# Kernel tuning notes

Hardware: AMD Instinct MI355X
Metric: run time of the kernel (lower is better)

## Reference

```python
import math
import jax, jax.numpy as jnp
import numpy as np

E = 1024
H = 16
D = E // H  # head_dim = 64
B, T = 4, 2048


def setup_inputs() -> dict:
    key = jax.random.key(0)
    ks = jax.random.split(key, 9)
    s = 1.0 / math.sqrt(E)
    inp = {
        "x": jax.random.normal(ks[0], (B, T, E), dtype=jnp.float32),
        "Wq": jax.random.uniform(ks[1], (E, E), jnp.float32, -s, s),
        "bq": jax.random.uniform(ks[2], (E,), jnp.float32, -s, s),
        "Wk": jax.random.uniform(ks[3], (E, E), jnp.float32, -s, s),
        "bk": jax.random.uniform(ks[4], (E,), jnp.float32, -s, s),
        "Wv": jax.random.uniform(ks[5], (E, E), jnp.float32, -s, s),
        "bv": jax.random.uniform(ks[6], (E,), jnp.float32, -s, s),
        "Wo": jax.random.uniform(ks[7], (E, E), jnp.float32, -s, s),
        "bo": jax.random.uniform(ks[8], (E,), jnp.float32, -s, s),
    }
    return inp


def reference(x, Wq, bq, Wk, bk, Wv, bv, Wo, bo):
    # Linear projections (torch Linear: y = x @ W.T + b)
    q = x @ Wq.T + bq
    k = x @ Wk.T + bk
    v = x @ Wv.T + bv
    # [B, T, E] -> [B, H, T, D]
    def split_heads(t):
        return t.reshape(B, T, H, D).transpose(0, 2, 1, 3)
    q, k, v = split_heads(q), split_heads(k), split_heads(v)
    # scaled dot-product attention; note scale uses head_dim (attention(self.head_dim))
    scores = jnp.einsum("bhqd,bhkd->bhqk", q, k) / math.sqrt(D)
    attn = jax.nn.softmax(scores, axis=-1)
    out = jnp.einsum("bhqk,bhkd->bhqd", attn, v)
    out = out.transpose(0, 2, 1, 3).reshape(B, T, E)
    return out @ Wo.T + bo
```

## Files before the change

### kernel.cpp

```cpp
#include <hip/hip_runtime.h>

typedef short bh8 __attribute__((ext_vector_type(8)));
typedef short bh4 __attribute__((ext_vector_type(4)));
typedef float f4 __attribute__((ext_vector_type(4)));
typedef _Float16 fh4 __attribute__((ext_vector_type(4)));
typedef __fp16 hp2 __attribute__((ext_vector_type(2)));
typedef unsigned int u32;

#if __has_builtin(__builtin_amdgcn_exp2f)
#define EXP2(x) __builtin_amdgcn_exp2f(x)
#else
#define EXP2(x) exp2f(x)
#endif

__device__ __forceinline__ short f2bf(float f) {
  unsigned u = __float_as_uint(f);
  u += 0x7FFFu + ((u >> 16) & 1u);
  return (short)(u >> 16);
}

__device__ __forceinline__ short f2fh(float f) {
  union { hp2 h2; u32 u; } cv;
  cv.h2 = __builtin_amdgcn_cvt_pkrtz(f, f);
  return (short)(cv.u & 0xffffu);
}

__device__ __forceinline__ void async16(const void* g, void* l) {
  __builtin_amdgcn_global_load_lds((const __attribute__((address_space(1))) void*)g,
                                   (__attribute__((address_space(3))) void*)l, 16, 0, 0);
}

__global__ void cvt_kernel(const float* __restrict__ in, short* __restrict__ out, int n4) {
  int i = blockIdx.x * blockDim.x + threadIdx.x;
  if (i < n4) {
    f4 v = *(const f4*)(in + (size_t)i * 4);
    bh4 o;
    o[0] = f2bf(v[0]); o[1] = f2bf(v[1]); o[2] = f2bf(v[2]); o[3] = f2bf(v[3]);
    *(bh4*)(out + (size_t)i * 4) = o;
  }
}

__global__ void cvt_w4(const float* __restrict__ w0, const float* __restrict__ w1,
                       const float* __restrict__ w2, const float* __restrict__ w3,
                       short* __restrict__ out, int n4_per) {
  const float* in = blockIdx.y == 0 ? w0 : blockIdx.y == 1 ? w1 : blockIdx.y == 2 ? w2 : w3;
  short* o = out + (size_t)blockIdx.y * (size_t)n4_per * 4;
  int i = blockIdx.x * blockDim.x + threadIdx.x;
  if (i < n4_per) {
    f4 v = *(const f4*)(in + (size_t)i * 4);
    bh4 q;
    q[0] = f2bf(v[0]); q[1] = f2bf(v[1]); q[2] = f2bf(v[2]); q[3] = f2bf(v[3]);
    *(bh4*)(o + (size_t)i * 4) = q;
  }
}

template <typename OutT, bool BROW, bool F16OUT>
__device__ __forceinline__ void gemm_body(const short* __restrict__ A, const short* __restrict__ Bw,
                                          const float* __restrict__ bias, OutT* __restrict__ C,
                                          int m0, int n0, int N, int K, float scale,
                                          short* a_lds, short* b_lds) {
  const int t = threadIdx.x;
  const int lane = t & 63, wave = t >> 6, quad = lane >> 4, l15 = lane & 15;
  const int mw = (wave >> 1) * 64, nw = (wave & 1) * 64;

  f4 acc[4][4];
#pragma unroll
  for (int i = 0; i < 4; ++i)
#pragma unroll
    for (int j = 0; j < 4; ++j) acc[i][j] = (f4){0.f, 0.f, 0.f, 0.f};

  for (int k0 = 0; k0 < K; k0 += 64) {
#pragma unroll
    for (int i = 0; i < 4; ++i) {
      int c = i * 256 + t;
      int m = c >> 3;
      int kq = (c & 7) ^ (m & 7);
      const short* ga = A + (size_t)(m0 + m) * K + k0 + kq * 8;
      const short* gb = Bw + (size_t)(n0 + m) * K + k0 + kq * 8;
      async16(ga, (char*)a_lds + (i * 256 + wave * 64) * 16);
      async16(gb, (char*)b_lds + (i * 256 + wave * 64) * 16);
    }
    __syncthreads();
#pragma unroll
    for (int s = 0; s < 2; ++s) {
      bh8 af[4], bfr[4];
#pragma unroll
      for (int ms = 0; ms < 4; ++ms) {
        int m = mw + ms * 16 + l15;
        int slot = m * 8 + ((quad + s * 4) ^ (m & 7));
        af[ms] = *(const bh8*)(a_lds + slot * 8);
      }
#pragma unroll
      for (int ns = 0; ns < 4; ++ns) {
        int n = nw + ns * 16 + l15;
        int slot = n * 8 + ((quad + s * 4) ^ (n & 7));
        bfr[ns] = *(const bh8*)(b_lds + slot * 8);
      }
#pragma unroll
      for (int ms = 0; ms < 4; ++ms)
#pragma unroll
        for (int ns = 0; ns < 4; ++ns)
          acc[ms][ns] = __builtin_amdgcn_mfma_f32_16x16x32_bf16(af[ms], bfr[ns], acc[ms][ns], 0, 0, 0);
    }
    __syncthreads();
  }
#pragma unroll
  for (int ns = 0; ns < 4; ++ns) {
    int col = n0 + nw + ns * 16 + l15;
    float bcol = BROW ? 0.f : bias[col & 1023];
#pragma unroll
    for (int ms = 0; ms < 4; ++ms) {
      int row = m0 + mw + ms * 16 + quad * 4;
#pragma unroll
      for (int r = 0; r < 4; ++r) {
        float bv = BROW ? bias[(row + r) & 1023] : bcol;
        float v = (acc[ms][ns][r] + bv) * scale;
        if (sizeof(OutT) == 2)
          ((short*)C)[(size_t)(row + r) * N + col] = F16OUT ? f2fh(v) : f2bf(v);
        else
          ((float*)C)[(size_t)(row + r) * N + col] = v;
      }
    }
  }
}

__global__ void __launch_bounds__(256) gemm_qkv(
    const short* __restrict__ xb, const short* __restrict__ W3,
    const float* __restrict__ bq, const float* __restrict__ bk, const float* __restrict__ bv,
    short* __restrict__ Qo, short* __restrict__ Ko, short* __restrict__ VTo, float qscale) {
  __shared__ __align__(16) short a_lds[128 * 64];
  __shared__ __align__(16) short b_lds[128 * 64];
  const int which = blockIdx.x >> 3;
  if (which == 2) {
    const short* Wv = W3 + (size_t)2 * 1024 * 1024;
    gemm_body<short, true, true>(Wv, xb, bv, VTo, (blockIdx.x & 7) * 128, blockIdx.y * 128,
                                 8192, 1024, 1.0f, a_lds, b_lds);
  } else {
    const short* Bw = W3 + (size_t)which * 1024 * 1024;
    const float* bias = which == 0 ? bq : bk;
    short* C = which == 0 ? Qo : Ko;
    float scale = which == 0 ? qscale : 1.0f;
    gemm_body<short, false, false>(xb, Bw, bias, C, blockIdx.y * 128, (blockIdx.x & 7) * 128,
                                   1024, 1024, scale, a_lds, b_lds);
  }
}

__global__ void __launch_bounds__(256) gemm_bt_f32(
    const short* __restrict__ A, const short* __restrict__ Bw,
    const float* __restrict__ bias, float* __restrict__ C) {
  __shared__ __align__(16) short a_lds[128 * 64];
  __shared__ __align__(16) short b_lds[128 * 64];
  gemm_body<float, false, false>(A, Bw, bias, C, blockIdx.y * 128, blockIdx.x * 128,
                                 1024, 1024, 1.0f, a_lds, b_lds);
}

__global__ void __launch_bounds__(256) attn_kernel(
    const short* __restrict__ Qb, const short* __restrict__ Kb,
    const short* __restrict__ VTb, short* __restrict__ AO) {
  __shared__ __align__(16) short k_lds[64 * 64];
  __shared__ __align__(16) short vt_lds[64 * 64];
  const int t = threadIdx.x, lane = t & 63, wave = t >> 6, quad = lane >> 4, l15 = lane & 15;
  const int b = blockIdx.y >> 4, h = blockIdx.y & 15;
  const int q0 = blockIdx.x * 128;
  const size_t baseq = ((size_t)b * 2048) * 1024 + (size_t)h * 64;
  const size_t basev = ((size_t)h * 64) * 8192 + (size_t)b * 2048;

  bh8 qf[2][2];
#pragma unroll
  for (int mi = 0; mi < 2; ++mi)
#pragma unroll
    for (int ks = 0; ks < 2; ++ks)
      qf[mi][ks] = *(const bh8*)(Qb + baseq + (size_t)(q0 + wave * 32 + mi * 16 + l15) * 1024 + ks * 32 + quad * 8);

  f4 O[2][4];
  float l_part[2] = {0.f, 0.f};
#pragma unroll
  for (int mi = 0; mi < 2; ++mi)
#pragma unroll
    for (int di = 0; di < 4; ++di) O[mi][di] = (f4){0.f, 0.f, 0.f, 0.f};

  for (int kt = 0; kt < 2048; kt += 64) {
    __syncthreads();
#pragma unroll
    for (int i = 0; i < 2; ++i) {
      int c = i * 256 + t;
      int kk = c >> 3;
      int dq = (c & 7) ^ (kk & 7);
      async16(Kb + baseq + (size_t)(kt + kk) * 1024 + dq * 8,
              (char*)k_lds + (i * 256 + wave * 64) * 16);
    }
#pragma unroll
    for (int i = 0; i < 2; ++i) {
      int c = i * 256 + t;
      int d = c >> 3;
      int kc = (c & 7) ^ (d & 7);
      async16(VTb + basev + (size_t)d * 8192 + kt + kc * 8,
              (char*)vt_lds + (i * 256 + wave * 64) * 16);
    }
    __syncthreads();

    f4 ST[4][2];
#pragma unroll
    for (int mK = 0; mK < 4; ++mK) {
      int key = mK * 16 + l15;
      bh8 ka0 = *(const bh8*)(k_lds + (key * 8 + (quad ^ (key & 7))) * 8);
      bh8 ka1 = *(const bh8*)(k_lds + (key * 8 + ((quad + 4) ^ (key & 7))) * 8);
#pragma unroll
      for (int mi = 0; mi < 2; ++mi) {
        f4 s = (f4){-16.f, -16.f, -16.f, -16.f};
        s = __builtin_amdgcn_mfma_f32_16x16x32_bf16(ka0, qf[mi][0], s, 0, 0, 0);
        s = __builtin_amdgcn_mfma_f32_16x16x32_bf16(ka1, qf[mi][1], s, 0, 0, 0);
        ST[mK][mi] = s;
      }
    }

    fh4 pa[4][2];
#pragma unroll
    for (int mi = 0; mi < 2; ++mi) {
      float lp = 0.f;
#pragma unroll
      for (int mK = 0; mK < 4; ++mK) {
        float p0 = EXP2(ST[mK][mi][0]);
        float p1 = EXP2(ST[mK][mi][1]);
        float p2 = EXP2(ST[mK][mi][2]);
        float p3 = EXP2(ST[mK][mi][3]);
        lp += (p0 + p1) + (p2 + p3);
        hp2 lo = __builtin_amdgcn_cvt_pkrtz(p0, p1);
        hp2 hi = __builtin_amdgcn_cvt_pkrtz(p2, p3);
        fh4 pv;
        pv[0] = (_Float16)lo[0]; pv[1] = (_Float16)lo[1];
        pv[2] = (_Float16)hi[0]; pv[3] = (_Float16)hi[1];
        pa[mK][mi] = pv;
      }
      l_part[mi] += lp;
    }

#pragma unroll
    for (int di = 0; di < 4; ++di) {
      int d = di * 16 + l15;
#pragma unroll
      for (int mK = 0; mK < 4; ++mK) {
        int kc = mK * 2 + (quad >> 1);
        fh4 vb = *(const fh4*)(vt_lds + (d * 8 + (kc ^ (d & 7))) * 8 + (quad & 1) * 4);
#pragma unroll
        for (int mi = 0; mi < 2; ++mi)
          O[mi][di] = __builtin_amdgcn_mfma_f32_16x16x16f16(pa[mK][mi], vb, O[mi][di], 0, 0, 0);
      }
    }
  }

#pragma unroll
  for (int mi = 0; mi < 2; ++mi) {
    float l0 = l_part[mi];
    l0 += __shfl_xor(l0, 16);
    l0 += __shfl_xor(l0, 32);
    float rl[4];
#pragma unroll
    for (int r = 0; r < 4; ++r) {
      float lb = __shfl(l0, quad * 4 + r);
      rl[r] = __builtin_amdgcn_rcpf(lb);
    }
#pragma unroll
    for (int di = 0; di < 4; ++di)
#pragma unroll
      for (int r = 0; r < 4; ++r) {
        int row = q0 + wave * 32 + mi * 16 + quad * 4 + r;
        AO[baseq + (size_t)row * 1024 + di * 16 + l15] = f2bf(O[mi][di][r] * rl[r]);
      }
  }
}

extern "C" void kernel_launch(void* const* d_in, const int* in_sizes, int n_in,
                              void* d_out, int out_size, void* d_ws, size_t ws_size,
                              hipStream_t stream) {
  const float* x  = (const float*)d_in[0];
  const float* Wq = (const float*)d_in[1];
  const float* bq = (const float*)d_in[2];
  const float* Wk = (const float*)d_in[3];
  const float* bk = (const float*)d_in[4];
  const float* Wv = (const float*)d_in[5];
  const float* bv = (const float*)d_in[6];
  const float* Wo = (const float*)d_in[7];
  const float* bo = (const float*)d_in[8];
  float* out = (float*)d_out;

  const int M = 8192, E = 1024;
  const size_t NX = (size_t)M * E;
  const size_t NW = (size_t)E * E;

  short* ws  = (short*)d_ws;
  short* xb  = ws;
  short* wqb = xb + NX;
  short* wob = wqb + 3 * NW;
  short* qb  = wob + NW;
  short* kb  = qb + NX;
  short* vt  = kb + NX;
  short* aob = xb;

  cvt_kernel<<<dim3((unsigned)(NX / 1024)), 256, 0, stream>>>(x, xb, (int)(NX / 4));
  cvt_w4<<<dim3((unsigned)(NW / 1024), 4), 256, 0, stream>>>(Wq, Wk, Wv, Wo, wqb, (int)(NW / 4));

  const float qscale = 0.18033688011112042f;
  gemm_qkv<<<dim3(24, 64), 256, 0, stream>>>(xb, wqb, bq, bk, bv, qb, kb, vt, qscale);

  attn_kernel<<<dim3(16, 64), 256, 0, stream>>>(qb, kb, vt, aob);

  gemm_bt_f32<<<dim3(8, 64), 256, 0, stream>>>(aob, wob, bo, out);
}
```

Before: 300.6 us.

## Use bf16 16x16x32 MFMA for PV via LDS-staged P, double query rows per block

```diff
diff --git a/kernel.cpp b/kernel.cpp
--- a/kernel.cpp
+++ b/kernel.cpp
@@ -3,9 +3,8 @@
 typedef short bh8 __attribute__((ext_vector_type(8)));
 typedef short bh4 __attribute__((ext_vector_type(4)));
 typedef float f4 __attribute__((ext_vector_type(4)));
-typedef _Float16 fh4 __attribute__((ext_vector_type(4)));
-typedef __fp16 hp2 __attribute__((ext_vector_type(2)));
 typedef unsigned int u32;
+typedef u32 u32x2 __attribute__((ext_vector_type(2)));
 
 #if __has_builtin(__builtin_amdgcn_exp2f)
 #define EXP2(x) __builtin_amdgcn_exp2f(x)
@@ -17,12 +16,6 @@
   unsigned u = __float_as_uint(f);
   u += 0x7FFFu + ((u >> 16) & 1u);
   return (short)(u >> 16);
-}
-
-__device__ __forceinline__ short f2fh(float f) {
-  union { hp2 h2; u32 u; } cv;
-  cv.h2 = __builtin_amdgcn_cvt_pkrtz(f, f);
-  return (short)(cv.u & 0xffffu);
 }
 
 __device__ __forceinline__ void async16(const void* g, void* l) {
@@ -54,7 +47,7 @@
   }
 }
 
-template <typename OutT, bool BROW, bool F16OUT>
+template <typename OutT, bool BROW>
 __device__ __forceinline__ void gemm_body(const short* __restrict__ A, const short* __restrict__ Bw,
                                           const float* __restrict__ bias, OutT* __restrict__ C,
                                           int m0, int n0, int N, int K, float scale,
@@ -116,7 +109,7 @@
         float bv = BROW ? bias[(row + r) & 1023] : bcol;
         float v = (acc[ms][ns][r] + bv) * scale;
         if (sizeof(OutT) == 2)
-          ((short*)C)[(size_t)(row + r) * N + col] = F16OUT ? f2fh(v) : f2bf(v);
+          ((short*)C)[(size_t)(row + r) * N + col] = f2bf(v);
         else
           ((float*)C)[(size_t)(row + r) * N + col] = v;
       }
@@ -133,15 +126,15 @@
   const int which = blockIdx.x >> 3;
   if (which == 2) {
     const short* Wv = W3 + (size_t)2 * 1024 * 1024;
-    gemm_body<short, true, true>(Wv, xb, bv, VTo, (blockIdx.x & 7) * 128, blockIdx.y * 128,
-                                 8192, 1024, 1.0f, a_lds, b_lds);
+    gemm_body<short, true>(Wv, xb, bv, VTo, (blockIdx.x & 7) * 128, blockIdx.y * 128,
+                           8192, 1024, 1.0f, a_lds, b_lds);
   } else {
     const short* Bw = W3 + (size_t)which * 1024 * 1024;
     const float* bias = which == 0 ? bq : bk;
     short* C = which == 0 ? Qo : Ko;
     float scale = which == 0 ? qscale : 1.0f;
-    gemm_body<short, false, false>(xb, Bw, bias, C, blockIdx.y * 128, (blockIdx.x & 7) * 128,
-                                   1024, 1024, scale, a_lds, b_lds);
+    gemm_body<short, false>(xb, Bw, bias, C, blockIdx.y * 128, (blockIdx.x & 7) * 128,
+                            1024, 1024, scale, a_lds, b_lds);
   }
 }
 
@@ -150,8 +143,8 @@
     const float* __restrict__ bias, float* __restrict__ C) {
   __shared__ __align__(16) short a_lds[128 * 64];
   __shared__ __align__(16) short b_lds[128 * 64];
-  gemm_body<float, false, false>(A, Bw, bias, C, blockIdx.y * 128, blockIdx.x * 128,
-                                 1024, 1024, 1.0f, a_lds, b_lds);
+  gemm_body<float, false>(A, Bw, bias, C, blockIdx.y * 128, blockIdx.x * 128,
+                          1024, 1024, 1.0f, a_lds, b_lds);
 }
 
 __global__ void __launch_bounds__(256) attn_kernel(
@@ -159,23 +152,24 @@
     const short* __restrict__ VTb, short* __restrict__ AO) {
   __shared__ __align__(16) short k_lds[64 * 64];
   __shared__ __align__(16) short vt_lds[64 * 64];
+  __shared__ __align__(16) short p_lds[4][64 * 72];
   const int t = threadIdx.x, lane = t & 63, wave = t >> 6, quad = lane >> 4, l15 = lane & 15;
   const int b = blockIdx.y >> 4, h = blockIdx.y & 15;
-  const int q0 = blockIdx.x * 128;
+  const int q0 = blockIdx.x * 256;
   const size_t baseq = ((size_t)b * 2048) * 1024 + (size_t)h * 64;
   const size_t basev = ((size_t)h * 64) * 8192 + (size_t)b * 2048;
 
-  bh8 qf[2][2];
-#pragma unroll
-  for (int mi = 0; mi < 2; ++mi)
+  bh8 qf[4][2];
+#pragma unroll
+  for (int mi = 0; mi < 4; ++mi)
 #pragma unroll
     for (int ks = 0; ks < 2; ++ks)
-      qf[mi][ks] = *(const bh8*)(Qb + baseq + (size_t)(q0 + wave * 32 + mi * 16 + l15) * 1024 + ks * 32 + quad * 8);
-
-  f4 O[2][4];
-  float l_part[2] = {0.f, 0.f};
-#pragma unroll
-  for (int mi = 0; mi < 2; ++mi)
+      qf[mi][ks] = *(const bh8*)(Qb + baseq + (size_t)(q0 + wave * 64 + mi * 16 + l15) * 1024 + ks * 32 + quad * 8);
+
+  f4 O[4][4];
+  float l_part[4] = {0.f, 0.f, 0.f, 0.f};
+#pragma unroll
+  for (int mi = 0; mi < 4; ++mi)
 #pragma unroll
     for (int di = 0; di < 4; ++di) O[mi][di] = (f4){0.f, 0.f, 0.f, 0.f};
 
@@ -199,14 +193,14 @@
     }
     __syncthreads();
 
-    f4 ST[4][2];
+    f4 ST[4][4];
 #pragma unroll
     for (int mK = 0; mK < 4; ++mK) {
       int key = mK * 16 + l15;
       bh8 ka0 = *(const bh8*)(k_lds + (key * 8 + (quad ^ (key & 7))) * 8);
       bh8 ka1 = *(const bh8*)(k_lds + (key * 8 + ((quad + 4) ^ (key & 7))) * 8);
 #pragma unroll
-      for (int mi = 0; mi < 2; ++mi) {
+      for (int mi = 0; mi < 4; ++mi) {
         f4 s = (f4){-16.f, -16.f, -16.f, -16.f};
         s = __builtin_amdgcn_mfma_f32_16x16x32_bf16(ka0, qf[mi][0], s, 0, 0, 0);
         s = __builtin_amdgcn_mfma_f32_16x16x32_bf16(ka1, qf[mi][1], s, 0, 0, 0);
@@ -214,9 +208,8 @@
       }
     }
 
-    fh4 pa[4][2];
-#pragma unroll
-    for (int mi = 0; mi < 2; ++mi) {
+#pragma unroll
+    for (int mi = 0; mi < 4; ++mi) {
       float lp = 0.f;
 #pragma unroll
       for (int mK = 0; mK < 4; ++mK) {
@@ -225,32 +218,37 @@
         float p2 = EXP2(ST[mK][mi][2]);
         float p3 = EXP2(ST[mK][mi][3]);
         lp += (p0 + p1) + (p2 + p3);
-        hp2 lo = __builtin_amdgcn_cvt_pkrtz(p0, p1);
-        hp2 hi = __builtin_amdgcn_cvt_pkrtz(p2, p3);
-        fh4 pv;
-        pv[0] = (_Float16)lo[0]; pv[1] = (_Float16)lo[1];
-        pv[2] = (_Float16)hi[0]; pv[3] = (_Float16)hi[1];
-        pa[mK][mi] = pv;
+        u32 d0 = __builtin_amdgcn_perm(__float_as_uint(p1), __float_as_uint(p0), 0x07060302u);
+        u32 d1 = __builtin_amdgcn_perm(__float_as_uint(p3), __float_as_uint(p2), 0x07060302u);
+        u32x2 dd = {d0, d1};
+        *(u32x2*)(&p_lds[wave][(mi * 16 + l15) * 72 + mK * 16 + quad * 4]) = dd;
       }
       l_part[mi] += lp;
     }
 
+    bh8 pa[4][2];
+#pragma unroll
+    for (int mi = 0; mi < 4; ++mi)
+#pragma unroll
+      for (int ks = 0; ks < 2; ++ks)
+        pa[mi][ks] = *(const bh8*)(&p_lds[wave][(mi * 16 + l15) * 72 + ks * 32 + quad * 8]);
 #pragma unroll
     for (int di = 0; di < 4; ++di) {
       int d = di * 16 + l15;
-#pragma unroll
-      for (int mK = 0; mK < 4; ++mK) {
-        int kc = mK * 2 + (quad >> 1);
-        fh4 vb = *(const fh4*)(vt_lds + (d * 8 + (kc ^ (d & 7))) * 8 + (quad & 1) * 4);
-#pragma unroll
-        for (int mi = 0; mi < 2; ++mi)
-          O[mi][di] = __builtin_amdgcn_mfma_f32_16x16x16f16(pa[mK][mi], vb, O[mi][di], 0, 0, 0);
-      }
-    }
-  }
-
-#pragma unroll
-  for (int mi = 0; mi < 2; ++mi) {
+      bh8 vb0 = *(const bh8*)(vt_lds + (d * 8 + (quad ^ (d & 7))) * 8);
+      bh8 vb1 = *(const bh8*)(vt_lds + (d * 8 + ((quad + 4) ^ (d & 7))) * 8);
+#pragma unroll
+      for (int mi = 0; mi < 4; ++mi) {
+        f4 o = O[mi][di];
+        o = __builtin_amdgcn_mfma_f32_16x16x32_bf16(pa[mi][0], vb0, o, 0, 0, 0);
+        o = __builtin_amdgcn_mfma_f32_16x16x32_bf16(pa[mi][1], vb1, o, 0, 0, 0);
+        O[mi][di] = o;
+      }
+    }
+  }
+
+#pragma unroll
+  for (int mi = 0; mi < 4; ++mi) {
     float l0 = l_part[mi];
     l0 += __shfl_xor(l0, 16);
     l0 += __shfl_xor(l0, 32);
@@ -264,7 +262,7 @@
     for (int di = 0; di < 4; ++di)
 #pragma unroll
       for (int r = 0; r < 4; ++r) {
-        int row = q0 + wave * 32 + mi * 16 + quad * 4 + r;
+        int row = q0 + wave * 64 + mi * 16 + quad * 4 + r;
         AO[baseq + (size_t)row * 1024 + di * 16 + l15] = f2bf(O[mi][di][r] * rl[r]);
       }
   }
@@ -303,7 +301,7 @@
   const float qscale = 0.18033688011112042f;
   gemm_qkv<<<dim3(24, 64), 256, 0, stream>>>(xb, wqb, bq, bk, bv, qb, kb, vt, qscale);
 
-  attn_kernel<<<dim3(16, 64), 256, 0, stream>>>(qb, kb, vt, aob);
+  attn_kernel<<<dim3(8, 64), 256, 0, stream>>>(qb, kb, vt, aob);
 
   gemm_bt_f32<<<dim3(8, 64), 256, 0, stream>>>(aob, wob, bo, out);
 }
```

New measurement: 331.3 us. 1.1x slower.
